# Performance work log

Measured on AMD Instinct MI355X. Metric: run time of the kernel, lower is better.

## Reference

```python
import jax, jax.numpy as jnp
import numpy as np

QUERY_SIZE = 512
KEY_SIZE = 512
VALUE_SIZE = 512
HIDDEN = 128


def setup_inputs() -> dict:
    key = jax.random.key(0)
    ks = jax.random.split(key, 9)
    b, t_q, t_k = 8, 128, 512
    query = jax.random.normal(ks[0], (b, t_q, QUERY_SIZE), dtype=jnp.float32)
    keys = jax.random.normal(ks[1], (b, t_k, KEY_SIZE), dtype=jnp.float32)
    values = jax.random.normal(ks[2], (b, t_k, VALUE_SIZE), dtype=jnp.float32)
    # torch nn.Linear init ~ U(-1/sqrt(fan_in), 1/sqrt(fan_in)); scale-matched normals are fine
    sq = 1.0 / np.sqrt(QUERY_SIZE)
    sk = 1.0 / np.sqrt(KEY_SIZE)
    sh = 1.0 / np.sqrt(HIDDEN)
    Wq = jax.random.uniform(ks[3], (HIDDEN, QUERY_SIZE), jnp.float32, -sq, sq)
    bq = jax.random.uniform(ks[4], (HIDDEN,), jnp.float32, -sq, sq)
    Wk = jax.random.uniform(ks[5], (HIDDEN, KEY_SIZE), jnp.float32, -sk, sk)
    bk = jax.random.uniform(ks[6], (HIDDEN,), jnp.float32, -sk, sk)
    Wo = jax.random.uniform(ks[7], (1, HIDDEN), jnp.float32, -sh, sh)
    bo = jax.random.uniform(ks[8], (1,), jnp.float32, -sh, sh)
    return {"query": query, "keys": keys, "values": values,
            "Wq": Wq, "bq": bq, "Wk": Wk, "bk": bk, "Wo": Wo, "bo": bo}


def reference(query, keys, values, Wq, bq, Wk, bk, Wo, bo):
    # Bahdanau additive attention: att_ij = Wo @ tanh(Wq q_i + Wk k_j + bq + bk) + bo
    # Project once per position (mathematically identical to the expanded per-pair Linear).
    q_proj = jnp.einsum('bqn,hn->bqh', query, Wq) + bq          # b x t_q x h
    k_proj = jnp.einsum('bkn,hn->bkh', keys, Wk) + bk           # b x t_k x h
    hid = jnp.tanh(q_proj[:, :, None, :] + k_proj[:, None, :, :])  # b x t_q x t_k x h
    scores = jnp.einsum('bqkh,h->bqk', hid, Wo[0]) + bo[0]       # b x t_q x t_k
    attn = jax.nn.softmax(scores, axis=2)
    context = jnp.einsum('bqk,bkv->bqv', attn, values)           # b x t_q x n_v
    return context, attn
```

## Files before the change

### kernel.cpp

```cpp
#include <hip/hip_runtime.h>


#define B_    8
#define TQ_   128
#define TK_   512
#define NIN_  512
#define H_    128
#define NV_   512
#define NQR   (B_*TQ_)
#define NROWS (NQR + B_*TK_)

#define C2_   2.8853900817779268f
#define L2E_  1.4426950408889634f

__device__ __forceinline__ float fexp2(float x){ return __builtin_amdgcn_exp2f(x); }
__device__ __forceinline__ float frcp (float x){ return __builtin_amdgcn_rcpf(x); }

__global__ __launch_bounds__(256, 5) void proj_kernel(
        const float* __restrict__ query, const float* __restrict__ keys,
        const float* __restrict__ Wq, const float* __restrict__ Wk,
        float* __restrict__ psum, int kper) {
    __shared__ float at[32][18];
    __shared__ float wt[32][132];
    const int tid = threadIdx.x;
    const int r0  = blockIdx.x * 16;
    const float* in; const float* W;
    if (r0 < NQR) { in = query + (size_t)r0 * NIN_;         W = Wq; }
    else          { in = keys  + (size_t)(r0 - NQR) * NIN_; W = Wk; }

    const int r2 = (tid >> 5) * 2;
    const int h4 = (tid & 31) * 4;
    const int ar  = tid >> 4;
    const int ak2 = (tid & 15) * 2;
    const int wr  = tid >> 3;
    const int wkq = (tid & 7) * 4;
    const int kb0 = blockIdx.y * kper;
    const int nc  = kper >> 5;

    const float* pA  = in + ar * NIN_ + kb0 + ak2;
    const float* pW0 = W + (wr     ) * NIN_ + kb0 + wkq;
    const float* pW1 = W + (wr + 32) * NIN_ + kb0 + wkq;
    const float* pW2 = W + (wr + 64) * NIN_ + kb0 + wkq;
    const float* pW3 = W + (wr + 96) * NIN_ + kb0 + wkq;

    float2 af  = *(const float2*)pA;
    float4 wf0 = *(const float4*)pW0;
    float4 wf1 = *(const float4*)pW1;
    float4 wf2 = *(const float4*)pW2;
    float4 wf3 = *(const float4*)pW3;

    float acc[2][4] = {{0.f,0.f,0.f,0.f},{0.f,0.f,0.f,0.f}};

    for (int c = 0; c < nc; ++c) {
        __syncthreads();
        at[ak2+0][ar] = af.x;  at[ak2+1][ar] = af.y;
        wt[wkq+0][wr   ] = wf0.x; wt[wkq+1][wr   ] = wf0.y;
        wt[wkq+2][wr   ] = wf0.z; wt[wkq+3][wr   ] = wf0.w;
        wt[wkq+0][wr+32] = wf1.x; wt[wkq+1][wr+32] = wf1.y;
        wt[wkq+2][wr+32] = wf1.z; wt[wkq+3][wr+32] = wf1.w;
        wt[wkq+0][wr+64] = wf2.x; wt[wkq+1][wr+64] = wf2.y;
        wt[wkq+2][wr+64] = wf2.z; wt[wkq+3][wr+64] = wf2.w;
        wt[wkq+0][wr+96] = wf3.x; wt[wkq+1][wr+96] = wf3.y;
        wt[wkq+2][wr+96] = wf3.z; wt[wkq+3][wr+96] = wf3.w;
        __syncthreads();
        if (c + 1 < nc) {
            pA += 32; pW0 += 32; pW1 += 32; pW2 += 32; pW3 += 32;
            af  = *(const float2*)pA;
            wf0 = *(const float4*)pW0; wf1 = *(const float4*)pW1;
            wf2 = *(const float4*)pW2; wf3 = *(const float4*)pW3;
        }
#pragma unroll 8
        for (int kk = 0; kk < 32; ++kk) {
            float2 a = *(const float2*)&at[kk][r2];
            float4 w = *(const float4*)&wt[kk][h4];
            acc[0][0] = fmaf(a.x, w.x, acc[0][0]);
            acc[0][1] = fmaf(a.x, w.y, acc[0][1]);
            acc[0][2] = fmaf(a.x, w.z, acc[0][2]);
            acc[0][3] = fmaf(a.x, w.w, acc[0][3]);
            acc[1][0] = fmaf(a.y, w.x, acc[1][0]);
            acc[1][1] = fmaf(a.y, w.y, acc[1][1]);
            acc[1][2] = fmaf(a.y, w.z, acc[1][2]);
            acc[1][3] = fmaf(a.y, w.w, acc[1][3]);
        }
    }

    float* op = psum + ((size_t)blockIdx.y * NROWS + r0) * H_;
#pragma unroll
    for (int i = 0; i < 2; ++i) {
        float4 o = {acc[i][0], acc[i][1], acc[i][2], acc[i][3]};
        *(float4*)&op[(r2 + i) * H_ + h4] = o;
    }
}

__global__ __launch_bounds__(256, 4) void reduce_kernel(
        const float* __restrict__ psum, const float* __restrict__ bq,
        const float* __restrict__ bk, float* __restrict__ qp,
        float* __restrict__ kpT) {
    __shared__ float lt[128][17];
    const int tid = threadIdx.x;
    const int r0  = blockIdx.x * 16;
    const bool isq = (r0 < NQR);
    const float* bias = isq ? bq : bk;

#pragma unroll
    for (int p = 0; p < 2; ++p) {
        const int j = tid + p * 256;
        const int row = j >> 5, hq = (j & 31) * 4;
        const float4 b4 = *(const float4*)&bias[hq];
        float4 s = b4;
#pragma unroll
        for (int sp = 0; sp < 4; ++sp) {
            float4 v = *(const float4*)&psum[((size_t)sp * NROWS + r0 + row) * H_ + hq];
            s.x += v.x; s.y += v.y; s.z += v.z; s.w += v.w;
        }
        if (isq) {
            *(float4*)&qp[(size_t)(r0 + row) * H_ + hq] = s;
        } else {
            lt[hq + 0][row] = s.x * C2_; lt[hq + 1][row] = s.y * C2_;
            lt[hq + 2][row] = s.z * C2_; lt[hq + 3][row] = s.w * C2_;
        }
    }
    if (!isq) {
        __syncthreads();
        const int b  = (r0 - NQR) >> 9;
        const int k0 = (r0 - NQR) & 511;
#pragma unroll
        for (int p = 0; p < 2; ++p) {
            const int j = tid + p * 256;
            const int h = j >> 2, kq = (j & 3) * 4;
            float4 o = {lt[h][kq], lt[h][kq + 1], lt[h][kq + 2], lt[h][kq + 3]};
            *(float4*)&kpT[((size_t)b * H_ + h) * TK_ + k0 + kq] = o;
        }
    }
}

__global__ __launch_bounds__(256, 4) void scores_kernel(
        const float* __restrict__ qp, const float* __restrict__ kpT,
        const float* __restrict__ Wo, const float* __restrict__ bo,
        float* __restrict__ out_attn) {
    __shared__ float qs2[2][H_];
    __shared__ float w2[H_];
    __shared__ float sc[2][TK_];

    const int tid = threadIdx.x;
    const int b   = blockIdx.y;
    const int q0  = blockIdx.x * 2;
    const int lane = tid & 63;

    qs2[tid >> 7][tid & 127] =
        qp[(b * TQ_ + q0 + (tid >> 7)) * H_ + (tid & 127)] * C2_;
    if (tid < H_) w2[tid] = Wo[tid] * -2.0f;
    __syncthreads();

    float sw = w2[lane] + w2[lane + 64];
#pragma unroll
    for (int m = 1; m < 64; m <<= 1) sw += __shfl_xor(sw, m);
    const float sbase = bo[0] - 0.5f * sw;

    const int k4 = (tid & 127) * 4;
    const int qi = tid >> 7;
    const float* pk = kpT + (size_t)b * H_ * TK_ + k4;
    float a0 = 0.f, a1 = 0.f, a2 = 0.f, a3 = 0.f;
#pragma unroll 4
    for (int h = 0; h < H_; ++h) {
        float4 kv = *(const float4*)pk;
        pk += TK_;
        const float qv = qs2[qi][h];
        const float wv = w2[h];
        a0 = fmaf(wv, frcp(fexp2(qv + kv.x) + 1.0f), a0);
        a1 = fmaf(wv, frcp(fexp2(qv + kv.y) + 1.0f), a1);
        a2 = fmaf(wv, frcp(fexp2(qv + kv.z) + 1.0f), a2);
        a3 = fmaf(wv, frcp(fexp2(qv + kv.w) + 1.0f), a3);
    }
    float4 sv = {a0 + sbase, a1 + sbase, a2 + sbase, a3 + sbase};
    *(float4*)&sc[qi][k4] = sv;
    __syncthreads();

    const int w = tid >> 6;
    if (w < 2) {
        float4 sA = *(const float4*)&sc[w][lane * 8];
        float4 sB = *(const float4*)&sc[w][lane * 8 + 4];
        float m = fmaxf(fmaxf(fmaxf(sA.x, sA.y), fmaxf(sA.z, sA.w)),
                        fmaxf(fmaxf(sB.x, sB.y), fmaxf(sB.z, sB.w)));
#pragma unroll
        for (int mask = 1; mask < 64; mask <<= 1) m = fmaxf(m, __shfl_xor(m, mask));
        float4 eA, eB;
        eA.x = fexp2((sA.x - m) * L2E_); eA.y = fexp2((sA.y - m) * L2E_);
        eA.z = fexp2((sA.z - m) * L2E_); eA.w = fexp2((sA.w - m) * L2E_);
        eB.x = fexp2((sB.x - m) * L2E_); eB.y = fexp2((sB.y - m) * L2E_);
        eB.z = fexp2((sB.z - m) * L2E_); eB.w = fexp2((sB.w - m) * L2E_);
        float s = eA.x + eA.y + eA.z + eA.w + eB.x + eB.y + eB.z + eB.w;
#pragma unroll
        for (int mask = 1; mask < 64; mask <<= 1) s += __shfl_xor(s, mask);
        float inv = frcp(s);
        eA.x *= inv; eA.y *= inv; eA.z *= inv; eA.w *= inv;
        eB.x *= inv; eB.y *= inv; eB.z *= inv; eB.w *= inv;
        float4* op = (float4*)&out_attn[(b * TQ_ + q0 + w) * TK_ + lane * 8];
        op[0] = eA; op[1] = eB;
    }
}

__global__ __launch_bounds__(256, 4) void context_kernel(
        const float* __restrict__ attn, const float* __restrict__ values,
        float* __restrict__ outc) {
    __shared__ float at[32][20];
    __shared__ float vt[32][132];

    const int tid = threadIdx.x;
    const int b   = blockIdx.y;
    const int q0  = (blockIdx.x >> 2) * 16;
    const int v0  = (blockIdx.x & 3) * 128;

    const int tx = tid & 31, ty = tid >> 5;
    const int v4 = tx * 4,   r2 = ty * 2;
    const int ar = tid >> 3, akq = (tid & 7) * 4;
    const int vk = tid >> 5;

    const float* pAt = attn + (size_t)(b * TQ_ + q0 + ar) * TK_ + akq;
    const float* pV0 = values + (size_t)(b * TK_ + vk     ) * NV_ + v0 + v4;
    const float* pV1 = values + (size_t)(b * TK_ + vk +  8) * NV_ + v0 + v4;
    const float* pV2 = values + (size_t)(b * TK_ + vk + 16) * NV_ + v0 + v4;
    const float* pV3 = values + (size_t)(b * TK_ + vk + 24) * NV_ + v0 + v4;

    float4 af = {0.f,0.f,0.f,0.f};
    if (tid < 128) af = *(const float4*)pAt;
    float4 vf0 = *(const float4*)pV0;
    float4 vf1 = *(const float4*)pV1;
    float4 vf2 = *(const float4*)pV2;
    float4 vf3 = *(const float4*)pV3;

    float acc[2][4] = {{0.f,0.f,0.f,0.f},{0.f,0.f,0.f,0.f}};

    for (int c = 0; c < 16; ++c) {
        __syncthreads();
        if (tid < 128) {
            at[akq+0][ar] = af.x; at[akq+1][ar] = af.y;
            at[akq+2][ar] = af.z; at[akq+3][ar] = af.w;
        }
        *(float4*)&vt[vk     ][v4] = vf0;
        *(float4*)&vt[vk +  8][v4] = vf1;
        *(float4*)&vt[vk + 16][v4] = vf2;
        *(float4*)&vt[vk + 24][v4] = vf3;
        __syncthreads();
        if (c + 1 < 16) {
            pAt += 32; pV0 += 32 * NV_; pV1 += 32 * NV_;
            pV2 += 32 * NV_; pV3 += 32 * NV_;
            if (tid < 128) af = *(const float4*)pAt;
            vf0 = *(const float4*)pV0; vf1 = *(const float4*)pV1;
            vf2 = *(const float4*)pV2; vf3 = *(const float4*)pV3;
        }
#pragma unroll 8
        for (int kk = 0; kk < 32; ++kk) {
            float2 a = *(const float2*)&at[kk][r2];
            float4 v = *(const float4*)&vt[kk][v4];
            acc[0][0] = fmaf(a.x, v.x, acc[0][0]);
            acc[0][1] = fmaf(a.x, v.y, acc[0][1]);
            acc[0][2] = fmaf(a.x, v.z, acc[0][2]);
            acc[0][3] = fmaf(a.x, v.w, acc[0][3]);
            acc[1][0] = fmaf(a.y, v.x, acc[1][0]);
            acc[1][1] = fmaf(a.y, v.y, acc[1][1]);
            acc[1][2] = fmaf(a.y, v.z, acc[1][2]);
            acc[1][3] = fmaf(a.y, v.w, acc[1][3]);
        }
    }
    float4 o0 = {acc[0][0], acc[0][1], acc[0][2], acc[0][3]};
    float4 o1 = {acc[1][0], acc[1][1], acc[1][2], acc[1][3]};
    *(float4*)&outc[(size_t)(b * TQ_ + q0 + r2 + 0) * NV_ + v0 + v4] = o0;
    *(float4*)&outc[(size_t)(b * TQ_ + q0 + r2 + 1) * NV_ + v0 + v4] = o1;
}

extern "C" void kernel_launch(void* const* d_in, const int* in_sizes, int n_in,
                              void* d_out, int out_size, void* d_ws, size_t ws_size,
                              hipStream_t stream) {
    const float* query  = (const float*)d_in[0];
    const float* keys   = (const float*)d_in[1];
    const float* values = (const float*)d_in[2];
    const float* Wq     = (const float*)d_in[3];
    const float* bq     = (const float*)d_in[4];
    const float* Wk     = (const float*)d_in[5];
    const float* bk     = (const float*)d_in[6];
    const float* Wo     = (const float*)d_in[7];
    const float* bo     = (const float*)d_in[8];

    float* out_ctx  = (float*)d_out;
    float* out_attn = out_ctx + B_ * TQ_ * NV_;
    float* qp   = (float*)d_ws;
    float* kpT  = qp + (size_t)NQR * H_;
    float* psum = kpT + (size_t)B_ * H_ * TK_;

    proj_kernel<<<dim3(NROWS / 16, 4), 256, 0, stream>>>(
        query, keys, Wq, Wk, psum, NIN_ / 4);
    reduce_kernel<<<NROWS / 16, 256, 0, stream>>>(psum, bq, bk, qp, kpT);
    scores_kernel<<<dim3(TQ_ / 2, B_), 256, 0, stream>>>(qp, kpT, Wo, bo, out_attn);
    context_kernel<<<dim3(32, B_), 256, 0, stream>>>(out_attn, values, out_ctx);
}
```

Before: 68.92 us.

## Retile projection, reduce and context kernels for different per-thread work and grid sizes

The projection GEMM drops to 128 threads per block, and each thread now computes a 4x4 output tile instead of 2x4. This raises register-level reuse but halves the thread count per block. The reduce kernel handles 8 rows per block instead of 16, doubling its grid. The context kernel shrinks to 8x64 tiles with 128 threads and a 2x2 per-thread tile, quadrupling the grid to fill more CUs at the cost of lower arithmetic intensity per thread.

```diff
diff --git a/kernel.cpp b/kernel.cpp
--- a/kernel.cpp
+++ b/kernel.cpp
@@ -16,11 +16,11 @@
 __device__ __forceinline__ float fexp2(float x){ return __builtin_amdgcn_exp2f(x); }
 __device__ __forceinline__ float frcp (float x){ return __builtin_amdgcn_rcpf(x); }
 
-__global__ __launch_bounds__(256, 5) void proj_kernel(
+__global__ __launch_bounds__(128, 4) void proj_kernel(
         const float* __restrict__ query, const float* __restrict__ keys,
         const float* __restrict__ Wq, const float* __restrict__ Wk,
         float* __restrict__ psum, int kper) {
-    __shared__ float at[32][18];
+    __shared__ float at[32][20];
     __shared__ float wt[32][132];
     const int tid = threadIdx.x;
     const int r0  = blockIdx.x * 16;
@@ -28,67 +28,84 @@
     if (r0 < NQR) { in = query + (size_t)r0 * NIN_;         W = Wq; }
     else          { in = keys  + (size_t)(r0 - NQR) * NIN_; W = Wk; }
 
-    const int r2 = (tid >> 5) * 2;
+    const int r4 = (tid >> 5) * 4;
     const int h4 = (tid & 31) * 4;
-    const int ar  = tid >> 4;
-    const int ak2 = (tid & 15) * 2;
-    const int wr  = tid >> 3;
-    const int wkq = (tid & 7) * 4;
+    const int sr  = tid >> 3;
+    const int skq = (tid & 7) * 4;
     const int kb0 = blockIdx.y * kper;
     const int nc  = kper >> 5;
 
-    const float* pA  = in + ar * NIN_ + kb0 + ak2;
-    const float* pW0 = W + (wr     ) * NIN_ + kb0 + wkq;
-    const float* pW1 = W + (wr + 32) * NIN_ + kb0 + wkq;
-    const float* pW2 = W + (wr + 64) * NIN_ + kb0 + wkq;
-    const float* pW3 = W + (wr + 96) * NIN_ + kb0 + wkq;
-
-    float2 af  = *(const float2*)pA;
-    float4 wf0 = *(const float4*)pW0;
-    float4 wf1 = *(const float4*)pW1;
-    float4 wf2 = *(const float4*)pW2;
-    float4 wf3 = *(const float4*)pW3;
-
-    float acc[2][4] = {{0.f,0.f,0.f,0.f},{0.f,0.f,0.f,0.f}};
+    const float* pA = in + sr * NIN_ + kb0 + skq;
+    const float* pW0 = W + (sr      ) * NIN_ + kb0 + skq;
+    const float* pW1 = W + (sr + 16 ) * NIN_ + kb0 + skq;
+    const float* pW2 = W + (sr + 32 ) * NIN_ + kb0 + skq;
+    const float* pW3 = W + (sr + 48 ) * NIN_ + kb0 + skq;
+    const float* pW4 = W + (sr + 64 ) * NIN_ + kb0 + skq;
+    const float* pW5 = W + (sr + 80 ) * NIN_ + kb0 + skq;
+    const float* pW6 = W + (sr + 96 ) * NIN_ + kb0 + skq;
+    const float* pW7 = W + (sr + 112) * NIN_ + kb0 + skq;
+
+    float4 af  = *(const float4*)pA;
+    float4 w0 = *(const float4*)pW0, w1 = *(const float4*)pW1;
+    float4 w2 = *(const float4*)pW2, w3 = *(const float4*)pW3;
+    float4 w4 = *(const float4*)pW4, w5 = *(const float4*)pW5;
+    float4 w6 = *(const float4*)pW6, w7 = *(const float4*)pW7;
+
+    float acc[4][4];
+#pragma unroll
+    for (int i = 0; i < 4; ++i)
+#pragma unroll
+        for (int j = 0; j < 4; ++j) acc[i][j] = 0.0f;
 
     for (int c = 0; c < nc; ++c) {
         __syncthreads();
-        at[ak2+0][ar] = af.x;  at[ak2+1][ar] = af.y;
-        wt[wkq+0][wr   ] = wf0.x; wt[wkq+1][wr   ] = wf0.y;
-        wt[wkq+2][wr   ] = wf0.z; wt[wkq+3][wr   ] = wf0.w;
-        wt[wkq+0][wr+32] = wf1.x; wt[wkq+1][wr+32] = wf1.y;
-        wt[wkq+2][wr+32] = wf1.z; wt[wkq+3][wr+32] = wf1.w;
-        wt[wkq+0][wr+64] = wf2.x; wt[wkq+1][wr+64] = wf2.y;
-        wt[wkq+2][wr+64] = wf2.z; wt[wkq+3][wr+64] = wf2.w;
-        wt[wkq+0][wr+96] = wf3.x; wt[wkq+1][wr+96] = wf3.y;
-        wt[wkq+2][wr+96] = wf3.z; wt[wkq+3][wr+96] = wf3.w;
+        at[skq+0][sr] = af.x; at[skq+1][sr] = af.y;
+        at[skq+2][sr] = af.z; at[skq+3][sr] = af.w;
+        wt[skq+0][sr    ] = w0.x; wt[skq+1][sr    ] = w0.y;
+        wt[skq+2][sr    ] = w0.z; wt[skq+3][sr    ] = w0.w;
+        wt[skq+0][sr+ 16] = w1.x; wt[skq+1][sr+ 16] = w1.y;
+        wt[skq+2][sr+ 16] = w1.z; wt[skq+3][sr+ 16] = w1.w;
+        wt[skq+0][sr+ 32] = w2.x; wt[skq+1][sr+ 32] = w2.y;
+        wt[skq+2][sr+ 32] = w2.z; wt[skq+3][sr+ 32] = w2.w;
+        wt[skq+0][sr+ 48] = w3.x; wt[skq+1][sr+ 48] = w3.y;
+        wt[skq+2][sr+ 48] = w3.z; wt[skq+3][sr+ 48] = w3.w;
+        wt[skq+0][sr+ 64] = w4.x; wt[skq+1][sr+ 64] = w4.y;
+        wt[skq+2][sr+ 64] = w4.z; wt[skq+3][sr+ 64] = w4.w;
+        wt[skq+0][sr+ 80] = w5.x; wt[skq+1][sr+ 80] = w5.y;
+        wt[skq+2][sr+ 80] = w5.z; wt[skq+3][sr+ 80] = w5.w;
+        wt[skq+0][sr+ 96] = w6.x; wt[skq+1][sr+ 96] = w6.y;
+        wt[skq+2][sr+ 96] = w6.z; wt[skq+3][sr+ 96] = w6.w;
+        wt[skq+0][sr+112] = w7.x; wt[skq+1][sr+112] = w7.y;
+        wt[skq+2][sr+112] = w7.z; wt[skq+3][sr+112] = w7.w;
         __syncthreads();
         if (c + 1 < nc) {
             pA += 32; pW0 += 32; pW1 += 32; pW2 += 32; pW3 += 32;
-            af  = *(const float2*)pA;
-            wf0 = *(const float4*)pW0; wf1 = *(const float4*)pW1;
-            wf2 = *(const float4*)pW2; wf3 = *(const float4*)pW3;
+            pW4 += 32; pW5 += 32; pW6 += 32; pW7 += 32;
+            af = *(const float4*)pA;
+            w0 = *(const float4*)pW0; w1 = *(const float4*)pW1;
+            w2 = *(const float4*)pW2; w3 = *(const float4*)pW3;
+            w4 = *(const float4*)pW4; w5 = *(const float4*)pW5;
+            w6 = *(const float4*)pW6; w7 = *(const float4*)pW7;
         }
 #pragma unroll 8
         for (int kk = 0; kk < 32; ++kk) {
-            float2 a = *(const float2*)&at[kk][r2];
+            float4 a = *(const float4*)&at[kk][r4];
             float4 w = *(const float4*)&wt[kk][h4];
-            acc[0][0] = fmaf(a.x, w.x, acc[0][0]);
-            acc[0][1] = fmaf(a.x, w.y, acc[0][1]);
-            acc[0][2] = fmaf(a.x, w.z, acc[0][2]);
-            acc[0][3] = fmaf(a.x, w.w, acc[0][3]);
-            acc[1][0] = fmaf(a.y, w.x, acc[1][0]);
-            acc[1][1] = fmaf(a.y, w.y, acc[1][1]);
-            acc[1][2] = fmaf(a.y, w.z, acc[1][2]);
-            acc[1][3] = fmaf(a.y, w.w, acc[1][3]);
+            float av[4] = {a.x, a.y, a.z, a.w};
+            float wv[4] = {w.x, w.y, w.z, w.w};
+#pragma unroll
+            for (int i = 0; i < 4; ++i)
+#pragma unroll
+                for (int j = 0; j < 4; ++j)
+                    acc[i][j] = fmaf(av[i], wv[j], acc[i][j]);
         }
     }
 
     float* op = psum + ((size_t)blockIdx.y * NROWS + r0) * H_;
 #pragma unroll
-    for (int i = 0; i < 2; ++i) {
+    for (int i = 0; i < 4; ++i) {
         float4 o = {acc[i][0], acc[i][1], acc[i][2], acc[i][3]};
-        *(float4*)&op[(r2 + i) * H_ + h4] = o;
+        *(float4*)&op[(r4 + i) * H_ + h4] = o;
     }
 }
 
@@ -96,41 +113,31 @@
         const float* __restrict__ psum, const float* __restrict__ bq,
         const float* __restrict__ bk, float* __restrict__ qp,
         float* __restrict__ kpT) {
-    __shared__ float lt[128][17];
+    __shared__ float lt[128][9];
     const int tid = threadIdx.x;
-    const int r0  = blockIdx.x * 16;
+    const int r0  = blockIdx.x * 8;
     const bool isq = (r0 < NQR);
     const float* bias = isq ? bq : bk;
 
-#pragma unroll
-    for (int p = 0; p < 2; ++p) {
-        const int j = tid + p * 256;
-        const int row = j >> 5, hq = (j & 31) * 4;
-        const float4 b4 = *(const float4*)&bias[hq];
-        float4 s = b4;
-#pragma unroll
-        for (int sp = 0; sp < 4; ++sp) {
-            float4 v = *(const float4*)&psum[((size_t)sp * NROWS + r0 + row) * H_ + hq];
-            s.x += v.x; s.y += v.y; s.z += v.z; s.w += v.w;
-        }
-        if (isq) {
-            *(float4*)&qp[(size_t)(r0 + row) * H_ + hq] = s;
-        } else {
-            lt[hq + 0][row] = s.x * C2_; lt[hq + 1][row] = s.y * C2_;
-            lt[hq + 2][row] = s.z * C2_; lt[hq + 3][row] = s.w * C2_;
-        }
-    }
-    if (!isq) {
+    const int row = tid >> 5, hq = (tid & 31) * 4;
+    const float4 b4 = *(const float4*)&bias[hq];
+    float4 s = b4;
+#pragma unroll
+    for (int sp = 0; sp < 4; ++sp) {
+        float4 v = *(const float4*)&psum[((size_t)sp * NROWS + r0 + row) * H_ + hq];
+        s.x += v.x; s.y += v.y; s.z += v.z; s.w += v.w;
+    }
+    if (isq) {
+        *(float4*)&qp[(size_t)(r0 + row) * H_ + hq] = s;
+    } else {
+        lt[hq + 0][row] = s.x * C2_; lt[hq + 1][row] = s.y * C2_;
+        lt[hq + 2][row] = s.z * C2_; lt[hq + 3][row] = s.w * C2_;
         __syncthreads();
         const int b  = (r0 - NQR) >> 9;
         const int k0 = (r0 - NQR) & 511;
-#pragma unroll
-        for (int p = 0; p < 2; ++p) {
-            const int j = tid + p * 256;
-            const int h = j >> 2, kq = (j & 3) * 4;
-            float4 o = {lt[h][kq], lt[h][kq + 1], lt[h][kq + 2], lt[h][kq + 3]};
-            *(float4*)&kpT[((size_t)b * H_ + h) * TK_ + k0 + kq] = o;
-        }
+        const int h = tid >> 1, kq = (tid & 1) * 4;
+        float4 o = {lt[h][kq], lt[h][kq + 1], lt[h][kq + 2], lt[h][kq + 3]};
+        *(float4*)&kpT[((size_t)b * H_ + h) * TK_ + k0 + kq] = o;
     }
 }
 
@@ -200,73 +207,71 @@
     }
 }
 
-__global__ __launch_bounds__(256, 4) void context_kernel(
+__global__ __launch_bounds__(128, 4) void context_kernel(
         const float* __restrict__ attn, const float* __restrict__ values,
         float* __restrict__ outc) {
-    __shared__ float at[32][20];
-    __shared__ float vt[32][132];
+    __shared__ float at[32][12];
+    __shared__ float vt[32][68];
 
     const int tid = threadIdx.x;
     const int b   = blockIdx.y;
-    const int q0  = (blockIdx.x >> 2) * 16;
-    const int v0  = (blockIdx.x & 3) * 128;
-
-    const int tx = tid & 31, ty = tid >> 5;
-    const int v4 = tx * 4,   r2 = ty * 2;
-    const int ar = tid >> 3, akq = (tid & 7) * 4;
-    const int vk = tid >> 5;
+    const int q0  = (blockIdx.x >> 3) * 8;
+    const int v0  = (blockIdx.x & 7) * 64;
+
+    const int v2 = (tid & 31) * 2;
+    const int q2 = (tid >> 5) * 2;
+    const int ar  = tid >> 3;
+    const int akq = (tid & 7) * 4;
+    const int vr  = tid >> 4;
+    const int vq  = (tid & 15) * 4;
 
     const float* pAt = attn + (size_t)(b * TQ_ + q0 + ar) * TK_ + akq;
-    const float* pV0 = values + (size_t)(b * TK_ + vk     ) * NV_ + v0 + v4;
-    const float* pV1 = values + (size_t)(b * TK_ + vk +  8) * NV_ + v0 + v4;
-    const float* pV2 = values + (size_t)(b * TK_ + vk + 16) * NV_ + v0 + v4;
-    const float* pV3 = values + (size_t)(b * TK_ + vk + 24) * NV_ + v0 + v4;
+    const float* pV0 = values + (size_t)(b * TK_ + vr     ) * NV_ + v0 + vq;
+    const float* pV1 = values + (size_t)(b * TK_ + vr +  8) * NV_ + v0 + vq;
+    const float* pV2 = values + (size_t)(b * TK_ + vr + 16) * NV_ + v0 + vq;
+    const float* pV3 = values + (size_t)(b * TK_ + vr + 24) * NV_ + v0 + vq;
 
     float4 af = {0.f,0.f,0.f,0.f};
-    if (tid < 128) af = *(const float4*)pAt;
+    if (tid < 64) af = *(const float4*)pAt;
     float4 vf0 = *(const float4*)pV0;
     float4 vf1 = *(const float4*)pV1;
     float4 vf2 = *(const float4*)pV2;
     float4 vf3 = *(const float4*)pV3;
 
-    float acc[2][4] = {{0.f,0.f,0.f,0.f},{0.f,0.f,0.f,0.f}};
+    float acc[2][2] = {{0.f,0.f},{0.f,0.f}};
 
     for (int c = 0; c < 16; ++c) {
         __syncthreads();
-        if (tid < 128) {
+        if (tid < 64) {
             at[akq+0][ar] = af.x; at[akq+1][ar] = af.y;
             at[akq+2][ar] = af.z; at[akq+3][ar] = af.w;
         }
-        *(float4*)&vt[vk     ][v4] = vf0;
-        *(float4*)&vt[vk +  8][v4] = vf1;
-        *(float4*)&vt[vk + 16][v4] = vf2;
-        *(float4*)&vt[vk + 24][v4] = vf3;
+        *(float4*)&vt[vr     ][vq] = vf0;
+        *(float4*)&vt[vr +  8][vq] = vf1;
+        *(float4*)&vt[vr + 16][vq] = vf2;
+        *(float4*)&vt[vr + 24][vq] = vf3;
         __syncthreads();
         if (c + 1 < 16) {
             pAt += 32; pV0 += 32 * NV_; pV1 += 32 * NV_;
             pV2 += 32 * NV_; pV3 += 32 * NV_;
-            if (tid < 128) af = *(const float4*)pAt;
+            if (tid < 64) af = *(const float4*)pAt;
             vf0 = *(const float4*)pV0; vf1 = *(const float4*)pV1;
             vf2 = *(const float4*)pV2; vf3 = *(const float4*)pV3;
         }
 #pragma unroll 8
         for (int kk = 0; kk < 32; ++kk) {
-            float2 a = *(const float2*)&at[kk][r2];
-            float4 v = *(const float4*)&vt[kk][v4];
+            float2 a = *(const float2*)&at[kk][q2];
+            float2 v = *(const float2*)&vt[kk][v2];
             acc[0][0] = fmaf(a.x, v.x, acc[0][0]);
             acc[0][1] = fmaf(a.x, v.y, acc[0][1]);
-            acc[0][2] = fmaf(a.x, v.z, acc[0][2]);
-            acc[0][3] = fmaf(a.x, v.w, acc[0][3]);
             acc[1][0] = fmaf(a.y, v.x, acc[1][0]);
             acc[1][1] = fmaf(a.y, v.y, acc[1][1]);
-            acc[1][2] = fmaf(a.y, v.z, acc[1][2]);
-            acc[1][3] = fmaf(a.y, v.w, acc[1][3]);
-        }
-    }
-    float4 o0 = {acc[0][0], acc[0][1], acc[0][2], acc[0][3]};
-    float4 o1 = {acc[1][0], acc[1][1], acc[1][2], acc[1][3]};
-    *(float4*)&outc[(size_t)(b * TQ_ + q0 + r2 + 0) * NV_ + v0 + v4] = o0;
-    *(float4*)&outc[(size_t)(b * TQ_ + q0 + r2 + 1) * NV_ + v0 + v4] = o1;
+        }
+    }
+    float2 o0 = {acc[0][0], acc[0][1]};
+    float2 o1 = {acc[1][0], acc[1][1]};
+    *(float2*)&outc[(size_t)(b * TQ_ + q0 + q2 + 0) * NV_ + v0 + v2] = o0;
+    *(float2*)&outc[(size_t)(b * TQ_ + q0 + q2 + 1) * NV_ + v0 + v2] = o1;
 }
 
 extern "C" void kernel_launch(void* const* d_in, const int* in_sizes, int n_in,
@@ -288,9 +293,9 @@
     float* kpT  = qp + (size_t)NQR * H_;
     float* psum = kpT + (size_t)B_ * H_ * TK_;
 
-    proj_kernel<<<dim3(NROWS / 16, 4), 256, 0, stream>>>(
+    proj_kernel<<<dim3(NROWS / 16, 4), 128, 0, stream>>>(
         query, keys, Wq, Wk, psum, NIN_ / 4);
-    reduce_kernel<<<NROWS / 16, 256, 0, stream>>>(psum, bq, bk, qp, kpT);
+    reduce_kernel<<<NROWS / 8, 256, 0, stream>>>(psum, bq, bk, qp, kpT);
     scores_kernel<<<dim3(TQ_ / 2, B_), 256, 0, stream>>>(qp, kpT, Wo, bo, out_attn);
-    context_kernel<<<dim3(32, B_), 256, 0, stream>>>(out_attn, values, out_ctx);
-}
+    context_kernel<<<dim3(128, B_), 128, 0, stream>>>(out_attn, values, out_ctx);
+}
```

Result: no change. 69.17 us (+0.4%).
